# Optimization experiments

Hardware: AMD Instinct MI355X
Metric: run time of the kernel (lower is better)

## Reference

```python
import jax, jax.numpy as jnp
import numpy as np

EMB = 768
HS = 64
B, T = 4, 4096


def setup_inputs() -> dict:
    key = jax.random.key(0)
    ks = jax.random.split(key, 7)
    s = 1.0 / np.sqrt(EMB)
    return {
        "x": jax.random.normal(ks[0], (B, T, EMB), dtype=jnp.float32),
        "Wk": jax.random.normal(ks[1], (EMB, HS), dtype=jnp.float32) * s,
        "bk": jnp.zeros((HS,), dtype=jnp.float32),
        "Wq": jax.random.normal(ks[2], (EMB, HS), dtype=jnp.float32) * s,
        "bq": jnp.zeros((HS,), dtype=jnp.float32),
        "Wv": jax.random.normal(ks[3], (EMB, HS), dtype=jnp.float32) * s,
        "bv": jnp.zeros((HS,), dtype=jnp.float32),
    }


def reference(x, Wk, bk, Wq, bq, Wv, bv):
    # Linear projections: (B, T, emb) @ (emb, hs) + bias -> (B, T, hs)
    k = x @ Wk + bk
    q = x @ Wq + bq
    v = x @ Wv + bv
    # NOTE: original code computes key @ query^T (k on the left), no 1/sqrt(hs) scaling.
    att = jnp.einsum("bth,bsh->bts", k, q)  # (B, T, T)
    causal = jnp.tril(jnp.ones((T, T), dtype=bool))  # (T, T)
    att = jnp.where(causal, att, -jnp.inf)
    wei = jax.nn.softmax(att, axis=-1)
    return jnp.einsum("bts,bsh->bth", wei, v)  # (B, T, hs)
```

## Files before the change

kernel.cpp:

```cpp
#include <hip/hip_runtime.h>
#include <cmath>

static constexpr int EMB  = 768;
static constexpr int HS   = 64;
static constexpr int NB   = 4;
static constexpr int SEQ  = 4096;
static constexpr int MTOT = NB * SEQ;
static constexpr int SPLITS = 8;

typedef __attribute__((ext_vector_type(8))) short  short8x;
typedef __attribute__((ext_vector_type(4))) float  float4x;
typedef __attribute__((ext_vector_type(4))) unsigned short ushort4x;

__device__ inline unsigned short rne16(float f) {
    unsigned u = __builtin_bit_cast(unsigned, f);
    unsigned r = u + 0x7FFFu + ((u >> 16) & 1u);
    return (unsigned short)(r >> 16);
}
__device__ inline float bf2f(unsigned short h) {
    return __builtin_bit_cast(float, ((unsigned)h) << 16);
}

__global__ __launch_bounds__(256) void convert_w(
    const float* __restrict__ Wk, const float* __restrict__ Wq, const float* __restrict__ Wv,
    unsigned short* __restrict__ wpk)
{
    const int t    = blockIdx.x * 256 + threadIdx.x;
    const int lane = t & 63;
    const int rest = t >> 6;
    const int nng  = rest % 12;
    const int kcp  = rest / 12;
    const int kc   = kcp % 24;
    const int p    = kcp / 24;
    const int which= nng >> 2;
    const int nn   = nng & 3;
    const float* W = (which == 0) ? Wk : (which == 1) ? Wq : Wv;
    const int col  = nn * 16 + (lane & 15);
    const int kr   = kc * 32 + (lane >> 4) * 8;

    unsigned short o[8];
    #pragma unroll
    for (int j = 0; j < 8; ++j) {
        float w = W[(size_t)(kr + j) * HS + col];
        unsigned short h = rne16(w);
        o[j] = (p == 0) ? h : rne16(w - bf2f(h));
    }
    size_t base = ((size_t)((p * 24 + kc) * 12 + nng) * 64 + lane) * 8;
    *(short8x*)&wpk[base] = *(short8x*)o;
}

__global__ __launch_bounds__(256) void proj_kernel(
    const float* __restrict__ x,
    const unsigned short* __restrict__ wpk,
    const float* __restrict__ bk, const float* __restrict__ bq, const float* __restrict__ bv,
    unsigned short* __restrict__ khi, unsigned short* __restrict__ klo,
    unsigned short* __restrict__ qhi, unsigned short* __restrict__ qlo,
    unsigned short* __restrict__ vT)
{
    __shared__ unsigned short xh[2][32 * 72];
    __shared__ unsigned short xl[2][32 * 72];

    const int tid  = threadIdx.x;
    const int lane = tid & 63;
    const int w    = tid >> 6;
    const int l15  = lane & 15;
    const int quad = lane >> 4;
    const int row0 = blockIdx.x * 32;

    float4x acc[3][2] = {};
    float4  pre[2];

    #pragma unroll
    for (int it = 0; it < 2; ++it) {
        const int fi = tid + it * 256;
        const int r  = fi >> 4, c4 = (fi & 15) * 4;
        pre[it] = *(const float4*)&x[(size_t)(row0 + r) * EMB + 0 * 64 + c4];
    }
    #pragma unroll
    for (int it = 0; it < 2; ++it) {
        const int fi = tid + it * 256;
        const int r  = fi >> 4, c4 = (fi & 15) * 4;
        const float4 xv = pre[it];
        const unsigned short h0 = rne16(xv.x), h1 = rne16(xv.y),
                             h2 = rne16(xv.z), h3 = rne16(xv.w);
        ushort4x hv = {h0, h1, h2, h3};
        ushort4x lv = {rne16(xv.x - bf2f(h0)), rne16(xv.y - bf2f(h1)),
                       rne16(xv.z - bf2f(h2)), rne16(xv.w - bf2f(h3))};
        *(ushort4x*)&xh[0][r * 72 + c4] = hv;
        *(ushort4x*)&xl[0][r * 72 + c4] = lv;
    }

    for (int ch = 0; ch < 12; ++ch) {
        if (ch + 1 < 12) {
            #pragma unroll
            for (int it = 0; it < 2; ++it) {
                const int fi = tid + it * 256;
                const int r  = fi >> 4, c4 = (fi & 15) * 4;
                pre[it] = *(const float4*)&x[(size_t)(row0 + r) * EMB + (ch + 1) * 64 + c4];
            }
        }
        __syncthreads();
        const int buf = ch & 1;

        #pragma unroll
        for (int k0i = 0; k0i < 2; ++k0i) {
            const int k0 = k0i * 32;
            const int kc = ch * 2 + k0i;
            short8x ah[2], al[2];
            #pragma unroll
            for (int mi = 0; mi < 2; ++mi) {
                ah[mi] = *(const short8x*)&xh[buf][(mi * 16 + l15) * 72 + k0 + quad * 8];
                al[mi] = *(const short8x*)&xl[buf][(mi * 16 + l15) * 72 + k0 + quad * 8];
            }
            #pragma unroll
            for (int which = 0; which < 3; ++which) {
                const int nng = which * 4 + w;
                const short8x bh = *(const short8x*)&wpk[((size_t)((0 * 24 + kc) * 12 + nng) * 64 + lane) * 8];
                const short8x bl = *(const short8x*)&wpk[((size_t)((1 * 24 + kc) * 12 + nng) * 64 + lane) * 8];
                #pragma unroll
                for (int mi = 0; mi < 2; ++mi) {
                    acc[which][mi] = __builtin_amdgcn_mfma_f32_16x16x32_bf16(ah[mi], bh, acc[which][mi], 0, 0, 0);
                    acc[which][mi] = __builtin_amdgcn_mfma_f32_16x16x32_bf16(ah[mi], bl, acc[which][mi], 0, 0, 0);
                    acc[which][mi] = __builtin_amdgcn_mfma_f32_16x16x32_bf16(al[mi], bh, acc[which][mi], 0, 0, 0);
                }
            }
        }

        if (ch + 1 < 12) {
            const int nbuf = (ch + 1) & 1;
            #pragma unroll
            for (int it = 0; it < 2; ++it) {
                const int fi = tid + it * 256;
                const int r  = fi >> 4, c4 = (fi & 15) * 4;
                const float4 xv = pre[it];
                const unsigned short h0 = rne16(xv.x), h1 = rne16(xv.y),
                                     h2 = rne16(xv.z), h3 = rne16(xv.w);
                ushort4x hv = {h0, h1, h2, h3};
                ushort4x lv = {rne16(xv.x - bf2f(h0)), rne16(xv.y - bf2f(h1)),
                               rne16(xv.z - bf2f(h2)), rne16(xv.w - bf2f(h3))};
                *(ushort4x*)&xh[nbuf][r * 72 + c4] = hv;
                *(ushort4x*)&xl[nbuf][r * 72 + c4] = lv;
            }
        }
    }

    const int col = w * 16 + l15;
    const float bkv = bk[col], bqv = bq[col], bvv = bv[col];
    #pragma unroll
    for (int mi = 0; mi < 2; ++mi) {
        const int rbase = row0 + mi * 16 + quad * 4;
        #pragma unroll
        for (int r = 0; r < 4; ++r) {
            const float kv = acc[0][mi][r] + bkv;
            const unsigned short hk = rne16(kv);
            khi[(size_t)(rbase + r) * 64 + col] = hk;
            klo[(size_t)(rbase + r) * 64 + col] = rne16(kv - bf2f(hk));
            const float qv = acc[1][mi][r] + bqv;
            const unsigned short hq = rne16(qv);
            qhi[(size_t)(rbase + r) * 64 + col] = hq;
            qlo[(size_t)(rbase + r) * 64 + col] = rne16(qv - bf2f(hq));
        }
        const int b = rbase / SEQ;
        const int s = rbase % SEQ;
        ushort4x vv = {rne16(acc[2][mi][0] + bvv), rne16(acc[2][mi][1] + bvv),
                       rne16(acc[2][mi][2] + bvv), rne16(acc[2][mi][3] + bvv)};
        *(ushort4x*)&vT[((size_t)b * 64 + col) * SEQ + s] = vv;
    }
}

__global__ __launch_bounds__(256, 2) void attn_kernel(
    const unsigned short* __restrict__ khi, const unsigned short* __restrict__ klo,
    const unsigned short* __restrict__ qhi, const unsigned short* __restrict__ qlo,
    const unsigned short* __restrict__ vT,
    float* __restrict__ Opart, float* __restrict__ lpart)
{
    __shared__ unsigned short qh_s[64 * 72];
    __shared__ unsigned short ql_s[64 * 72];
    __shared__ unsigned short vt_s[64 * 72];
    __shared__ unsigned short psH[64 * 72];
    __shared__ unsigned short psL[64 * 72];

    const int tid  = threadIdx.x;
    const int lane = tid & 63;
    const int w    = tid >> 6;
    const int l15  = lane & 15;
    const int quad = lane >> 4;

    const int n  = blockIdx.x;
    const int sp = n & (SPLITS - 1);
    const int b  = (n >> 3) & (NB - 1);
    const int p  = n >> 5;
    const int jj[4] = {63 - p, 32 + p, 31 - p, p};
    const size_t rowb = (size_t)b * SEQ;

    float4x oacc[4][4] = {};
    float   l_r[4][4]  = {};

    const int sr = tid >> 3;
    const int c8 = (tid & 7) * 8;

    for (int ci = sp; ci <= jj[0]; ci += SPLITS) {
        const int s0 = ci * 64;
        __syncthreads();
        #pragma unroll
        for (int it = 0; it < 2; ++it) {
            const int r = sr + it * 32;
            *(short8x*)&qh_s[r * 72 + c8] = *(const short8x*)&qhi[(rowb + s0 + r) * 64 + c8];
            *(short8x*)&ql_s[r * 72 + c8] = *(const short8x*)&qlo[(rowb + s0 + r) * 64 + c8];
            *(short8x*)&vt_s[r * 72 + c8] = *(const short8x*)&vT[((size_t)b * 64 + r) * SEQ + s0 + c8];
        }
        __syncthreads();

        #pragma unroll
        for (int g = 0; g < 2; ++g) {
            const int idxH = g ? 1 : 0;
            const int idxL = g ? 2 : 3;
            const int jH = jj[idxH], jL = jj[idxL];
            const bool aH = (ci <= jH), aL = (ci <= jL);
            if (!aH && !aL) continue;

            short8x ahH[2], alH[2], ahL[2], alL[2];
            #pragma unroll
            for (int k0 = 0; k0 < 2; ++k0) {
                if (aH) {
                    const size_t rH = (rowb + jH * 64 + 16 * w + l15) * 64 + k0 * 32 + quad * 8;
                    ahH[k0] = *(const short8x*)&khi[rH];
                    alH[k0] = *(const short8x*)&klo[rH];
                }
                if (aL) {
                    const size_t rL = (rowb + jL * 64 + 16 * w + l15) * 64 + k0 * 32 + quad * 8;
                    ahL[k0] = *(const short8x*)&khi[rL];
                    alL[k0] = *(const short8x*)&klo[rL];
                }
            }

            float4x sH[4] = {}, sL[4] = {};
            __builtin_amdgcn_s_setprio(1);
            #pragma unroll
            for (int k0 = 0; k0 < 2; ++k0) {
                #pragma unroll
                for (int nn = 0; nn < 4; ++nn) {
                    const short8x bh = *(const short8x*)&qh_s[(nn * 16 + l15) * 72 + k0 * 32 + quad * 8];
                    const short8x bl = *(const short8x*)&ql_s[(nn * 16 + l15) * 72 + k0 * 32 + quad * 8];
                    if (aH) {
                        sH[nn] = __builtin_amdgcn_mfma_f32_16x16x32_bf16(ahH[k0], bh, sH[nn], 0, 0, 0);
                        sH[nn] = __builtin_amdgcn_mfma_f32_16x16x32_bf16(alH[k0], bh, sH[nn], 0, 0, 0);
                        sH[nn] = __builtin_amdgcn_mfma_f32_16x16x32_bf16(ahH[k0], bl, sH[nn], 0, 0, 0);
                    }
                    if (aL) {
                        sL[nn] = __builtin_amdgcn_mfma_f32_16x16x32_bf16(ahL[k0], bh, sL[nn], 0, 0, 0);
                        sL[nn] = __builtin_amdgcn_mfma_f32_16x16x32_bf16(alL[k0], bh, sL[nn], 0, 0, 0);
                        sL[nn] = __builtin_amdgcn_mfma_f32_16x16x32_bf16(ahL[k0], bl, sL[nn], 0, 0, 0);
                    }
                }
            }
            __builtin_amdgcn_s_setprio(0);

            #pragma unroll
            for (int hl = 0; hl < 2; ++hl) {
                const bool alive = hl ? aL : aH;
                if (!alive) continue;
                const int j   = hl ? jL : jH;
                const int idx = hl ? idxL : idxH;
                float4x* sc   = hl ? sL : sH;
                unsigned short* ps = hl ? psL : psH;
                if (ci == j) {
                    const int trow = j * 64 + 16 * w + quad * 4;
                    #pragma unroll
                    for (int nn = 0; nn < 4; ++nn) {
                        const int colg = s0 + nn * 16 + l15;
                        #pragma unroll
                        for (int r = 0; r < 4; ++r)
                            if (colg > trow + r) sc[nn][r] = -1e30f;
                    }
                }
                #pragma unroll
                for (int nn = 0; nn < 4; ++nn) {
                    #pragma unroll
                    for (int r = 0; r < 4; ++r) {
                        const float e = __expf(fminf(sc[nn][r], 80.0f));
                        const unsigned short h = rne16(e);
                        l_r[idx][r] += bf2f(h);
                        ps[(16 * w + quad * 4 + r) * 72 + nn * 16 + l15] = h;
                    }
                }
            }

            __builtin_amdgcn_s_setprio(1);
            #pragma unroll
            for (int k0 = 0; k0 < 2; ++k0) {
                short8x paH, paL;
                if (aH) paH = *(const short8x*)&psH[(16 * w + l15) * 72 + k0 * 32 + quad * 8];
                if (aL) paL = *(const short8x*)&psL[(16 * w + l15) * 72 + k0 * 32 + quad * 8];
                #pragma unroll
                for (int nn = 0; nn < 4; ++nn) {
                    const short8x vb = *(const short8x*)&vt_s[(nn * 16 + l15) * 72 + k0 * 32 + quad * 8];
                    if (aH) oacc[idxH][nn] = __builtin_amdgcn_mfma_f32_16x16x32_bf16(paH, vb, oacc[idxH][nn], 0, 0, 0);
                    if (aL) oacc[idxL][nn] = __builtin_amdgcn_mfma_f32_16x16x32_bf16(paL, vb, oacc[idxL][nn], 0, 0, 0);
                }
            }
            __builtin_amdgcn_s_setprio(0);
        }
    }

    #pragma unroll
    for (int idx = 0; idx < 4; ++idx) {
        const int j = jj[idx];
        if (idx == 3 && sp > p) continue;
        float lv[4];
        #pragma unroll
        for (int r = 0; r < 4; ++r) {
            float l = l_r[idx][r];
            l += __shfl_xor(l, 1);
            l += __shfl_xor(l, 2);
            l += __shfl_xor(l, 4);
            l += __shfl_xor(l, 8);
            lv[r] = l;
        }
        const size_t part = (size_t)(j * NB + b) * SPLITS + sp;
        float* Op = Opart + part * 4096;
        #pragma unroll
        for (int nn = 0; nn < 4; ++nn)
            #pragma unroll
            for (int r = 0; r < 4; ++r)
                Op[(16 * w + quad * 4 + r) * 64 + nn * 16 + l15] = oacc[idx][nn][r];
        if (l15 == 0) {
            #pragma unroll
            for (int r = 0; r < 4; ++r)
                lpart[part * 64 + 16 * w + quad * 4 + r] = lv[r];
        }
    }
}

__global__ __launch_bounds__(256) void combine_kernel(
    const float* __restrict__ Opart, const float* __restrict__ lpart,
    float* __restrict__ out)
{
    const int j   = blockIdx.x;
    const int b   = blockIdx.y;
    const int tid = threadIdx.x;
    const int row = blockIdx.z * 16 + (tid >> 4);
    const int c0  = (tid & 15) * 4;
    const size_t base = (size_t)(j * NB + b) * SPLITS;
    const int spmax = (j >= 16) ? SPLITS : ((j < SPLITS ? j : SPLITS - 1) + 1);

    float4 acc = {0.f, 0.f, 0.f, 0.f};
    float lsum = 0.f;
    for (int sp = 0; sp < spmax; ++sp) {
        lsum += lpart[(base + sp) * 64 + row];
        const float4 v = *(const float4*)&Opart[(base + sp) * 4096 + row * 64 + c0];
        acc.x += v.x; acc.y += v.y; acc.z += v.z; acc.w += v.w;
    }
    const float inv = 1.0f / lsum;
    float4 v;
    v.x = acc.x * inv; v.y = acc.y * inv; v.z = acc.z * inv; v.w = acc.w * inv;
    *(float4*)&out[((size_t)b * SEQ + j * 64 + row) * 64 + c0] = v;
}

extern "C" void kernel_launch(void* const* d_in, const int* in_sizes, int n_in,
                              void* d_out, int out_size, void* d_ws, size_t ws_size,
                              hipStream_t stream)
{
    const float* x  = (const float*)d_in[0];
    const float* Wk = (const float*)d_in[1];
    const float* bk = (const float*)d_in[2];
    const float* Wq = (const float*)d_in[3];
    const float* bq = (const float*)d_in[4];
    const float* Wv = (const float*)d_in[5];
    const float* bv = (const float*)d_in[6];
    float* out = (float*)d_out;

    const size_t NE = (size_t)MTOT * HS;
    unsigned short* khi = (unsigned short*)d_ws;
    unsigned short* klo = khi + NE;
    unsigned short* qhi = klo + NE;
    unsigned short* qlo = qhi + NE;
    unsigned short* vT  = qlo + NE;
    unsigned short* wpk = vT + NE;
    float* Opart = (float*)(wpk + 294912);
    float* lpart = Opart + (size_t)64 * NB * SPLITS * 4096;

    convert_w<<<144, 256, 0, stream>>>(Wk, Wq, Wv, wpk);
    proj_kernel<<<MTOT / 32, 256, 0, stream>>>(x, wpk, bk, bq, bv, khi, klo, qhi, qlo, vT);
    attn_kernel<<<16 * NB * SPLITS, 256, 0, stream>>>(khi, klo, qhi, qlo, vT, Opart, lpart);
    dim3 cgrid(64, NB, 4);
    combine_kernel<<<cgrid, 256, 0, stream>>>(Opart, lpart, out);
}
```

Measured before the change: 159.5 us.

## Double-buffer attention Q/V tiles and halve projection row tile

The attention kernel now stages Q-hi/Q-lo/V^T chunks in alternating shared-memory buffers, removing the leading barrier before each chunk load. The projection kernel processes 16 rows per block instead of 32, doubling the grid and adding a barrier before refilling the next x buffer. The intent is fewer synchronisation stalls and more parallelism in the projection. The cost is larger LDS use per attention block and more redundant weight loads per projection row.

```diff
diff --git a/kernel.cpp b/kernel.cpp
--- a/kernel.cpp
+++ b/kernel.cpp
@@ -57,47 +57,35 @@
     unsigned short* __restrict__ qhi, unsigned short* __restrict__ qlo,
     unsigned short* __restrict__ vT)
 {
-    __shared__ unsigned short xh[2][32 * 72];
-    __shared__ unsigned short xl[2][32 * 72];
+    __shared__ unsigned short xh[2][16 * 72];
+    __shared__ unsigned short xl[2][16 * 72];
 
     const int tid  = threadIdx.x;
     const int lane = tid & 63;
     const int w    = tid >> 6;
     const int l15  = lane & 15;
     const int quad = lane >> 4;
-    const int row0 = blockIdx.x * 32;
-
-    float4x acc[3][2] = {};
-    float4  pre[2];
-
-    #pragma unroll
-    for (int it = 0; it < 2; ++it) {
-        const int fi = tid + it * 256;
-        const int r  = fi >> 4, c4 = (fi & 15) * 4;
-        pre[it] = *(const float4*)&x[(size_t)(row0 + r) * EMB + 0 * 64 + c4];
-    }
-    #pragma unroll
-    for (int it = 0; it < 2; ++it) {
-        const int fi = tid + it * 256;
-        const int r  = fi >> 4, c4 = (fi & 15) * 4;
-        const float4 xv = pre[it];
-        const unsigned short h0 = rne16(xv.x), h1 = rne16(xv.y),
-                             h2 = rne16(xv.z), h3 = rne16(xv.w);
+    const int row0 = blockIdx.x * 16;
+
+    float4x acc[3] = {};
+    float4  pre;
+
+    {
+        const int r  = tid >> 4, c4 = (tid & 15) * 4;
+        pre = *(const float4*)&x[(size_t)(row0 + r) * EMB + 0 * 64 + c4];
+        const unsigned short h0 = rne16(pre.x), h1 = rne16(pre.y),
+                             h2 = rne16(pre.z), h3 = rne16(pre.w);
         ushort4x hv = {h0, h1, h2, h3};
-        ushort4x lv = {rne16(xv.x - bf2f(h0)), rne16(xv.y - bf2f(h1)),
-                       rne16(xv.z - bf2f(h2)), rne16(xv.w - bf2f(h3))};
+        ushort4x lv = {rne16(pre.x - bf2f(h0)), rne16(pre.y - bf2f(h1)),
+                       rne16(pre.z - bf2f(h2)), rne16(pre.w - bf2f(h3))};
         *(ushort4x*)&xh[0][r * 72 + c4] = hv;
         *(ushort4x*)&xl[0][r * 72 + c4] = lv;
     }
 
     for (int ch = 0; ch < 12; ++ch) {
         if (ch + 1 < 12) {
-            #pragma unroll
-            for (int it = 0; it < 2; ++it) {
-                const int fi = tid + it * 256;
-                const int r  = fi >> 4, c4 = (fi & 15) * 4;
-                pre[it] = *(const float4*)&x[(size_t)(row0 + r) * EMB + (ch + 1) * 64 + c4];
-            }
+            const int r  = tid >> 4, c4 = (tid & 15) * 4;
+            pre = *(const float4*)&x[(size_t)(row0 + r) * EMB + (ch + 1) * 64 + c4];
         }
         __syncthreads();
         const int buf = ch & 1;
@@ -106,66 +94,52 @@
         for (int k0i = 0; k0i < 2; ++k0i) {
             const int k0 = k0i * 32;
             const int kc = ch * 2 + k0i;
-            short8x ah[2], al[2];
-            #pragma unroll
-            for (int mi = 0; mi < 2; ++mi) {
-                ah[mi] = *(const short8x*)&xh[buf][(mi * 16 + l15) * 72 + k0 + quad * 8];
-                al[mi] = *(const short8x*)&xl[buf][(mi * 16 + l15) * 72 + k0 + quad * 8];
-            }
+            const short8x ah = *(const short8x*)&xh[buf][l15 * 72 + k0 + quad * 8];
+            const short8x al = *(const short8x*)&xl[buf][l15 * 72 + k0 + quad * 8];
             #pragma unroll
             for (int which = 0; which < 3; ++which) {
                 const int nng = which * 4 + w;
                 const short8x bh = *(const short8x*)&wpk[((size_t)((0 * 24 + kc) * 12 + nng) * 64 + lane) * 8];
                 const short8x bl = *(const short8x*)&wpk[((size_t)((1 * 24 + kc) * 12 + nng) * 64 + lane) * 8];
-                #pragma unroll
-                for (int mi = 0; mi < 2; ++mi) {
-                    acc[which][mi] = __builtin_amdgcn_mfma_f32_16x16x32_bf16(ah[mi], bh, acc[which][mi], 0, 0, 0);
-                    acc[which][mi] = __builtin_amdgcn_mfma_f32_16x16x32_bf16(ah[mi], bl, acc[which][mi], 0, 0, 0);
-                    acc[which][mi] = __builtin_amdgcn_mfma_f32_16x16x32_bf16(al[mi], bh, acc[which][mi], 0, 0, 0);
-                }
+                acc[which] = __builtin_amdgcn_mfma_f32_16x16x32_bf16(ah, bh, acc[which], 0, 0, 0);
+                acc[which] = __builtin_amdgcn_mfma_f32_16x16x32_bf16(ah, bl, acc[which], 0, 0, 0);
+                acc[which] = __builtin_amdgcn_mfma_f32_16x16x32_bf16(al, bh, acc[which], 0, 0, 0);
             }
         }
 
         if (ch + 1 < 12) {
             const int nbuf = (ch + 1) & 1;
-            #pragma unroll
-            for (int it = 0; it < 2; ++it) {
-                const int fi = tid + it * 256;
-                const int r  = fi >> 4, c4 = (fi & 15) * 4;
-                const float4 xv = pre[it];
-                const unsigned short h0 = rne16(xv.x), h1 = rne16(xv.y),
-                                     h2 = rne16(xv.z), h3 = rne16(xv.w);
-                ushort4x hv = {h0, h1, h2, h3};
-                ushort4x lv = {rne16(xv.x - bf2f(h0)), rne16(xv.y - bf2f(h1)),
-                               rne16(xv.z - bf2f(h2)), rne16(xv.w - bf2f(h3))};
-                *(ushort4x*)&xh[nbuf][r * 72 + c4] = hv;
-                *(ushort4x*)&xl[nbuf][r * 72 + c4] = lv;
-            }
+            const int r  = tid >> 4, c4 = (tid & 15) * 4;
+            const unsigned short h0 = rne16(pre.x), h1 = rne16(pre.y),
+                                 h2 = rne16(pre.z), h3 = rne16(pre.w);
+            ushort4x hv = {h0, h1, h2, h3};
+            ushort4x lv = {rne16(pre.x - bf2f(h0)), rne16(pre.y - bf2f(h1)),
+                           rne16(pre.z - bf2f(h2)), rne16(pre.w - bf2f(h3))};
+            __syncthreads();
+            *(ushort4x*)&xh[nbuf][r * 72 + c4] = hv;
+            *(ushort4x*)&xl[nbuf][r * 72 + c4] = lv;
         }
     }
 
     const int col = w * 16 + l15;
     const float bkv = bk[col], bqv = bq[col], bvv = bv[col];
+    const int rbase = row0 + quad * 4;
     #pragma unroll
-    for (int mi = 0; mi < 2; ++mi) {
-        const int rbase = row0 + mi * 16 + quad * 4;
-        #pragma unroll
-        for (int r = 0; r < 4; ++r) {
-            const float kv = acc[0][mi][r] + bkv;
-            const unsigned short hk = rne16(kv);
-            khi[(size_t)(rbase + r) * 64 + col] = hk;
-            klo[(size_t)(rbase + r) * 64 + col] = rne16(kv - bf2f(hk));
-            const float qv = acc[1][mi][r] + bqv;
-            const unsigned short hq = rne16(qv);
-            qhi[(size_t)(rbase + r) * 64 + col] = hq;
-            qlo[(size_t)(rbase + r) * 64 + col] = rne16(qv - bf2f(hq));
-        }
-        const int b = rbase / SEQ;
-        const int s = rbase % SEQ;
-        ushort4x vv = {rne16(acc[2][mi][0] + bvv), rne16(acc[2][mi][1] + bvv),
-                       rne16(acc[2][mi][2] + bvv), rne16(acc[2][mi][3] + bvv)};
-        *(ushort4x*)&vT[((size_t)b * 64 + col) * SEQ + s] = vv;
-    }
+    for (int r = 0; r < 4; ++r) {
+        const float kv = acc[0][r] + bkv;
+        const unsigned short hk = rne16(kv);
+        khi[(size_t)(rbase + r) * 64 + col] = hk;
+        klo[(size_t)(rbase + r) * 64 + col] = rne16(kv - bf2f(hk));
+        const float qv = acc[1][r] + bqv;
+        const unsigned short hq = rne16(qv);
+        qhi[(size_t)(rbase + r) * 64 + col] = hq;
+        qlo[(size_t)(rbase + r) * 64 + col] = rne16(qv - bf2f(hq));
+    }
+    const int b = rbase / SEQ;
+    const int s = rbase % SEQ;
+    ushort4x vv = {rne16(acc[2][0] + bvv), rne16(acc[2][1] + bvv),
+                   rne16(acc[2][2] + bvv), rne16(acc[2][3] + bvv)};
+    *(ushort4x*)&vT[((size_t)b * 64 + col) * SEQ + s] = vv;
 }
 
 __global__ __launch_bounds__(256, 2) void attn_kernel(
@@ -174,9 +148,9 @@
     const unsigned short* __restrict__ vT,
     float* __restrict__ Opart, float* __restrict__ lpart)
 {
-    __shared__ unsigned short qh_s[64 * 72];
-    __shared__ unsigned short ql_s[64 * 72];
-    __shared__ unsigned short vt_s[64 * 72];
+    __shared__ unsigned short qh_s[2][64 * 72];
+    __shared__ unsigned short ql_s[2][64 * 72];
+    __shared__ unsigned short vt_s[2][64 * 72];
     __shared__ unsigned short psH[64 * 72];
     __shared__ unsigned short psL[64 * 72];
 
@@ -199,17 +173,21 @@
     const int sr = tid >> 3;
     const int c8 = (tid & 7) * 8;
 
+    int cur = 0;
     for (int ci = sp; ci <= jj[0]; ci += SPLITS) {
         const int s0 = ci * 64;
-        __syncthreads();
         #pragma unroll
         for (int it = 0; it < 2; ++it) {
             const int r = sr + it * 32;
-            *(short8x*)&qh_s[r * 72 + c8] = *(const short8x*)&qhi[(rowb + s0 + r) * 64 + c8];
-            *(short8x*)&ql_s[r * 72 + c8] = *(const short8x*)&qlo[(rowb + s0 + r) * 64 + c8];
-            *(short8x*)&vt_s[r * 72 + c8] = *(const short8x*)&vT[((size_t)b * 64 + r) * SEQ + s0 + c8];
+            *(short8x*)&qh_s[cur][r * 72 + c8] = *(const short8x*)&qhi[(rowb + s0 + r) * 64 + c8];
+            *(short8x*)&ql_s[cur][r * 72 + c8] = *(const short8x*)&qlo[(rowb + s0 + r) * 64 + c8];
+            *(short8x*)&vt_s[cur][r * 72 + c8] = *(const short8x*)&vT[((size_t)b * 64 + r) * SEQ + s0 + c8];
         }
         __syncthreads();
+        const unsigned short* qhc = qh_s[cur];
+        const unsigned short* qlc = ql_s[cur];
+        const unsigned short* vtc = vt_s[cur];
+        cur ^= 1;
 
         #pragma unroll
         for (int g = 0; g < 2; ++g) {
@@ -240,8 +218,8 @@
             for (int k0 = 0; k0 < 2; ++k0) {
                 #pragma unroll
                 for (int nn = 0; nn < 4; ++nn) {
-                    const short8x bh = *(const short8x*)&qh_s[(nn * 16 + l15) * 72 + k0 * 32 + quad * 8];
-                    const short8x bl = *(const short8x*)&ql_s[(nn * 16 + l15) * 72 + k0 * 32 + quad * 8];
+                    const short8x bh = *(const short8x*)&qhc[(nn * 16 + l15) * 72 + k0 * 32 + quad * 8];
+                    const short8x bl = *(const short8x*)&qlc[(nn * 16 + l15) * 72 + k0 * 32 + quad * 8];
                     if (aH) {
                         sH[nn] = __builtin_amdgcn_mfma_f32_16x16x32_bf16(ahH[k0], bh, sH[nn], 0, 0, 0);
                         sH[nn] = __builtin_amdgcn_mfma_f32_16x16x32_bf16(alH[k0], bh, sH[nn], 0, 0, 0);
@@ -294,7 +272,7 @@
                 if (aL) paL = *(const short8x*)&psL[(16 * w + l15) * 72 + k0 * 32 + quad * 8];
                 #pragma unroll
                 for (int nn = 0; nn < 4; ++nn) {
-                    const short8x vb = *(const short8x*)&vt_s[(nn * 16 + l15) * 72 + k0 * 32 + quad * 8];
+                    const short8x vb = *(const short8x*)&vtc[(nn * 16 + l15) * 72 + k0 * 32 + quad * 8];
                     if (aH) oacc[idxH][nn] = __builtin_amdgcn_mfma_f32_16x16x32_bf16(paH, vb, oacc[idxH][nn], 0, 0, 0);
                     if (aL) oacc[idxL][nn] = __builtin_amdgcn_mfma_f32_16x16x32_bf16(paL, vb, oacc[idxL][nn], 0, 0, 0);
                 }
@@ -381,7 +359,7 @@
     float* lpart = Opart + (size_t)64 * NB * SPLITS * 4096;
 
     convert_w<<<144, 256, 0, stream>>>(Wk, Wq, Wv, wpk);
-    proj_kernel<<<MTOT / 32, 256, 0, stream>>>(x, wpk, bk, bq, bv, khi, klo, qhi, qlo, vT);
+    proj_kernel<<<MTOT / 16, 256, 0, stream>>>(x, wpk, bk, bq, bv, khi, klo, qhi, qlo, vT);
     attn_kernel<<<16 * NB * SPLITS, 256, 0, stream>>>(khi, klo, qhi, qlo, vT, Opart, lpart);
     dim3 cgrid(64, NB, 4);
     combine_kernel<<<cgrid, 256, 0, stream>>>(Opart, lpart, out);
```

Result: slower. 168.7 us (+5.8%).
